# Kernel tuning notes

Hardware: AMD Instinct MI355X
Metric: run time of the kernel (lower is better)

Reference implementation:

```python
import jax, jax.numpy as jnp
import numpy as np

B, S, H = 2, 2048, 2048
NH, NKV, HD = 32, 8, 64
ROPE_THETA = 10000.0


def _rope_cos_sin(seq_len, head_dim, dtype):
    inv_freq = 1.0 / (ROPE_THETA ** (jnp.arange(0, head_dim, 2, dtype=jnp.float32) / head_dim))
    pos = jnp.arange(seq_len, dtype=jnp.float32)
    freqs = jnp.outer(pos, inv_freq)                 # [S, HD/2]
    emb = jnp.concatenate([freqs, freqs], axis=-1)   # [S, HD]
    return jnp.cos(emb).astype(dtype), jnp.sin(emb).astype(dtype)


def _rotate_half(x):
    x1, x2 = jnp.split(x, 2, axis=-1)
    return jnp.concatenate([-x2, x1], axis=-1)


def setup_inputs() -> dict:
    key = jax.random.key(0)
    ks = jax.random.split(key, 5)
    sc = 0.02
    return {
        'hidden_states': jax.random.normal(ks[0], (B, S, H), dtype=jnp.float32),
        'attention_mask': jnp.ones((B, S), dtype=jnp.int32),
        'Wq': jax.random.normal(ks[1], (H, NH * HD), dtype=jnp.float32) * sc,
        'Wk': jax.random.normal(ks[2], (H, NKV * HD), dtype=jnp.float32) * sc,
        'Wv': jax.random.normal(ks[3], (H, NKV * HD), dtype=jnp.float32) * sc,
        'Wo': jax.random.normal(ks[4], (NH * HD, H), dtype=jnp.float32) * sc,
    }


def reference(hidden_states, attention_mask, Wq, Wk, Wv, Wo):
    b, s, _ = hidden_states.shape
    n_rep = NH // NKV
    q = (hidden_states @ Wq).reshape(b, s, NH, HD).transpose(0, 2, 1, 3)    # [b,NH,s,d]
    k = (hidden_states @ Wk).reshape(b, s, NKV, HD).transpose(0, 2, 1, 3)   # [b,NKV,s,d]
    v = (hidden_states @ Wv).reshape(b, s, NKV, HD).transpose(0, 2, 1, 3)

    cos, sin = _rope_cos_sin(s, HD, q.dtype)          # [s, d]
    cos, sin = cos[None, None], sin[None, None]
    q = q * cos + _rotate_half(q) * sin
    k = k * cos + _rotate_half(k) * sin

    # repeat_kv
    k = jnp.repeat(k, n_rep, axis=1)                  # [b,NH,s,d]
    v = jnp.repeat(v, n_rep, axis=1)

    min_val = jnp.finfo(q.dtype).min
    causal = jnp.where(jnp.triu(jnp.ones((s, s), dtype=bool), k=1), min_val, 0.0).astype(q.dtype)
    mask = causal[None, None]                         # [1,1,s,s]
    pad = (attention_mask == 0)[:, None, None, :]     # [b,1,1,s]
    mask = jnp.where(pad, min_val, mask)              # [b,1,s,s]

    scale = 1.0 / jnp.sqrt(jnp.asarray(HD, dtype=q.dtype))
    scores = jnp.einsum('bhqd,bhkd->bhqk', q, k) * scale + mask
    attn = jax.nn.softmax(scores, axis=-1)
    out = jnp.einsum('bhqk,bhkd->bhqd', attn, v)      # [b,NH,s,d]
    out = out.transpose(0, 2, 1, 3).reshape(b, s, NH * HD)
    return out @ Wo
```

## Files before the change

kernel.cpp:

```cpp
#include <hip/hip_runtime.h>
#include <hip/hip_bf16.h>
#include <math.h>

#define B_   2
#define S_   2048
#define H_   2048
#define NH_  32
#define NKV_ 8
#define HD_  64
#define M_   (B_*S_)
#define QCOLS (NH_*HD_)
#define KVCOLS (NKV_*HD_)

typedef __bf16 bf16x8 __attribute__((ext_vector_type(8)));
typedef short  short8_t __attribute__((ext_vector_type(8)));
typedef float  f32x4 __attribute__((ext_vector_type(4)));
typedef float  f32x16 __attribute__((ext_vector_type(16)));

__device__ __forceinline__ short f2bf(float f) {
  __hip_bfloat16 h = __float2bfloat16(f);
  union { __hip_bfloat16 h; short s; } u; u.h = h; return u.s;
}
__device__ __forceinline__ float bf2f(short s) {
  union { short s; __hip_bfloat16 h; } u; u.s = s;
  return __bfloat162float(u.h);
}

__device__ __forceinline__ unsigned cvt_pk_bf16(float a, float b) {
  unsigned r;
  asm("v_cvt_pk_bf16_f32 %0, %1, %2" : "=v"(r) : "v"(a), "v"(b));
  return r;
}

__device__ __forceinline__ void gload_lds16(const void* g, void* l) {
  __builtin_amdgcn_global_load_lds(
      (const __attribute__((address_space(1))) unsigned int*)g,
      (__attribute__((address_space(3))) unsigned int*)l, 16, 0, 0);
}


__global__ void convert_x_kernel(const float4* __restrict__ in, short* __restrict__ out, int n4) {
  int i = blockIdx.x * blockDim.x + threadIdx.x;
  if (i >= n4) return;
  float4 v = in[i];
  short4 o;
  o.x = f2bf(v.x); o.y = f2bf(v.y); o.z = f2bf(v.z); o.w = f2bf(v.w);
  *reinterpret_cast<short4*>(out + (size_t)i * 4) = o;
}

__global__ __launch_bounds__(256) void wtrans_kernel(const float* __restrict__ W,
                                                     short* __restrict__ Wt,
                                                     int K, int N) {
  __shared__ float tile[32][33];
  int n0 = blockIdx.x * 32, k0 = blockIdx.y * 32;
  int tx = threadIdx.x & 31, ty = threadIdx.x >> 5;
  #pragma unroll
  for (int j = 0; j < 32; j += 8)
    tile[ty + j][tx] = W[(size_t)(k0 + ty + j) * N + n0 + tx];
  __syncthreads();
  #pragma unroll
  for (int j = 0; j < 32; j += 8)
    Wt[(size_t)(n0 + ty + j) * K + k0 + tx] = f2bf(tile[tx][ty + j]);
}

__global__ void sincos_kernel(float2* __restrict__ tab) {
  int i = blockIdx.x * blockDim.x + threadIdx.x;
  int pos = i >> 5, f = i & 31;
  float inv = powf(10000.0f, -(float)f * (1.0f / 32.0f));
  float ang = (float)pos * inv;
  float s, c;
  sincosf(ang, &s, &c);
  tab[i] = make_float2(c, s);
}

template <int OUT_MODE>
__global__ __launch_bounds__(256, 2)
void gemm_db_kernel(const short* __restrict__ A, const short* __restrict__ Bt,
                    void* __restrict__ Cout, short* __restrict__ Vout,
                    const float2* __restrict__ tab, int M, int N, int K) {
  __shared__ short As[2][128 * 64];
  __shared__ short Bs[2][128 * 64];
  const int tid = threadIdx.x;
  const int lane = tid & 63, wave = tid >> 6;
  const int m0 = blockIdx.x * 128, n0 = blockIdx.y * 128;
  const int wm = (wave >> 1) * 64, wn = (wave & 1) * 64;
  const int lr = lane & 15, lk = (lane >> 4) * 8;
  const int srow = lane >> 3;
  const int scol = 8 * ((lane & 7) ^ srow);

  f32x4 acc[4][4];
  const f32x4 z = {0.f, 0.f, 0.f, 0.f};
  #pragma unroll
  for (int i = 0; i < 4; ++i)
    #pragma unroll
    for (int j = 0; j < 4; ++j) acc[i][j] = z;

  const int nt = K >> 6;

  auto stage = [&](int t, int buf) {
    const int kt = t << 6;
    #pragma unroll
    for (int i = 0; i < 4; ++i) {
      int chunk = wave * 4 + i;
      int row = chunk * 8 + srow;
      gload_lds16(&A[(size_t)(m0 + row) * K + kt + scol], &As[buf][chunk * 512]);
      gload_lds16(&Bt[(size_t)(n0 + row) * K + kt + scol], &Bs[buf][chunk * 512]);
    }
  };

  stage(0, 0);
  stage(1, 1);
  asm volatile("s_waitcnt vmcnt(8)" ::: "memory");
  __builtin_amdgcn_s_barrier();

  int aoff[4], boff[4];
  #pragma unroll
  for (int i = 0; i < 4; ++i) {
    int ra = wm + i * 16 + lr;
    int rb = wn + i * 16 + lr;
    aoff[i] = ra * 64 + (lk ^ ((ra & 7) << 3));
    boff[i] = rb * 64 + (lk ^ ((rb & 7) << 3));
  }

  for (int t = 0; t < nt; ++t) {
    const short* as = As[t & 1];
    const short* bs = Bs[t & 1];
    bf16x8 af[2][4], bfr[2][4];
    #pragma unroll
    for (int kh = 0; kh < 2; ++kh) {
      #pragma unroll
      for (int mi = 0; mi < 4; ++mi)
        af[kh][mi] = *reinterpret_cast<const bf16x8*>(&as[aoff[mi] ^ (kh * 32)]);
      #pragma unroll
      for (int ni = 0; ni < 4; ++ni)
        bfr[kh][ni] = *reinterpret_cast<const bf16x8*>(&bs[boff[ni] ^ (kh * 32)]);
    }
    #pragma unroll
    for (int kh = 0; kh < 2; ++kh)
      #pragma unroll
      for (int mi = 0; mi < 4; ++mi)
        #pragma unroll
        for (int ni = 0; ni < 4; ++ni)
          acc[mi][ni] = __builtin_amdgcn_mfma_f32_16x16x32_bf16(
              af[kh][mi], bfr[kh][ni], acc[mi][ni], 0, 0, 0);

    asm volatile("s_waitcnt lgkmcnt(0)" ::: "memory");
    __builtin_amdgcn_s_barrier();
    if (t + 2 < nt) {
      stage(t + 2, t & 1);
      asm volatile("s_waitcnt vmcnt(8)" ::: "memory");
    } else {
      asm volatile("s_waitcnt vmcnt(0)" ::: "memory");
    }
    __builtin_amdgcn_s_barrier();
  }

  const int r0 = (lane >> 4) * 4, cc = lane & 15;

  if (OUT_MODE == 1) {
    #pragma unroll
    for (int mi = 0; mi < 4; ++mi)
      #pragma unroll
      for (int ni = 0; ni < 4; ++ni)
        #pragma unroll
        for (int r = 0; r < 4; ++r) {
          int row = m0 + wm + mi * 16 + r0 + r;
          int col = n0 + wn + ni * 16 + cc;
          ((float*)Cout)[(size_t)row * N + col] = acc[mi][ni][r];
        }
  }

  if (OUT_MODE == 3) {
    #pragma unroll
    for (int mi = 0; mi < 4; ++mi)
      #pragma unroll
      for (int ni = 0; ni < 2; ++ni)
        #pragma unroll
        for (int r = 0; r < 4; ++r) {
          int row = m0 + wm + mi * 16 + r0 + r;
          int pos = row & (S_ - 1);
          int i = ni * 16 + cc;
          float2 cs = tab[pos * 32 + i];
          float a = acc[mi][ni][r], b = acc[mi][ni + 2][r];
          int col = n0 + wn + i;
          ((short*)Cout)[(size_t)row * QCOLS + col]      = f2bf((a * cs.x - b * cs.y) * 0.125f);
          ((short*)Cout)[(size_t)row * QCOLS + col + 32] = f2bf((b * cs.x + a * cs.y) * 0.125f);
        }
  }

  if (OUT_MODE == 5) {
    if (n0 + wn < 512) {
      #pragma unroll
      for (int mi = 0; mi < 4; ++mi)
        #pragma unroll
        for (int ni = 0; ni < 2; ++ni)
          #pragma unroll
          for (int r = 0; r < 4; ++r) {
            int row = m0 + wm + mi * 16 + r0 + r;
            int pos = row & (S_ - 1);
            int i = ni * 16 + cc;
            float2 cs = tab[pos * 32 + i];
            float a = acc[mi][ni][r], b = acc[mi][ni + 2][r];
            int col = n0 + wn + i;
            ((short*)Cout)[(size_t)row * KVCOLS + col]      = f2bf(a * cs.x - b * cs.y);
            ((short*)Cout)[(size_t)row * KVCOLS + col + 32] = f2bf(b * cs.x + a * cs.y);
          }
    } else {
      #pragma unroll
      for (int mi = 0; mi < 4; ++mi)
        #pragma unroll
        for (int ni = 0; ni < 4; ++ni) {
          int colv = n0 + wn + ni * 16 + cc - 512;
          int kvh = colv >> 6, d = colv & 63;
          int rowb = m0 + wm + mi * 16 + r0;
          int bb = rowb >> 11, s0 = rowb & (S_ - 1);
          short4 pk;
          pk.x = f2bf(acc[mi][ni][0]); pk.y = f2bf(acc[mi][ni][1]);
          pk.z = f2bf(acc[mi][ni][2]); pk.w = f2bf(acc[mi][ni][3]);
          *reinterpret_cast<short4*>(
              &Vout[(((size_t)(bb * NKV_ + kvh)) * 64 + d) * S_ + s0]) = pk;
        }
    }
  }
}

__global__ __launch_bounds__(512, 2)
void attn4_kernel(const short* __restrict__ Q, const short* __restrict__ Kc,
                  const short* __restrict__ Vtg, short* __restrict__ AO) {
  __shared__ short Ks[2][64 * 64];
  __shared__ short Vs[2][64 * 64];
  const int qt = (int)(gridDim.x - 1) - (int)blockIdx.x;
  const int h = blockIdx.y, b = blockIdx.z;
  const int hk = h >> 2;
  const int tid = threadIdx.x, lane = tid & 63, wave = tid >> 6;
  const int q0 = qt * 256;
  const int qw0 = q0 + wave * 32;
  const int l31 = lane & 31, l5 = lane >> 5;

  const short* Kbase = Kc + ((size_t)b * S_) * KVCOLS + hk * HD_;
  const short* Vbase = Vtg + ((size_t)(b * NKV_ + hk) * HD_) * S_;

  bf16x8 qf[4];
  {
    const short* qrow = Q + ((size_t)(b * S_ + qw0 + l31)) * QCOLS + h * HD_;
    #pragma unroll
    for (int kk = 0; kk < 4; ++kk)
      qf[kk] = *reinterpret_cast<const bf16x8*>(qrow + kk * 16 + l5 * 8);
  }

  const int r8 = lane >> 3;
  const int c8s = ((lane & 7) ^ r8) * 8;
  auto stageKV = [&](int t, int buf) {
    int row = wave * 8 + r8;
    gload_lds16(Kbase + (size_t)(t * 64 + row) * KVCOLS + c8s, &Ks[buf][wave * 512]);
    gload_lds16(Vbase + (size_t)row * S_ + t * 64 + c8s, &Vs[buf][wave * 512]);
  };

  f32x16 o0, o1;
  #pragma unroll
  for (int e = 0; e < 16; ++e) { o0[e] = 0.f; o1[e] = 0.f; }
  float lsum = 0.f;

  const int nt = qt * 4 + 4;
  const int rowx = (l31 & 7);

  stageKV(0, 0);
  stageKV(1, 1);
  asm volatile("s_waitcnt vmcnt(2)" ::: "memory");
  __builtin_amdgcn_s_barrier();

  for (int t = 0; t < nt; ++t) {
    const short* ks = Ks[t & 1];
    const short* vs = Vs[t & 1];
    const bool active = (t * 64 <= qw0 + 31);

    if (active) {
      f32x16 sa[2];
      #pragma unroll
      for (int e = 0; e < 16; ++e) { sa[0][e] = 0.f; sa[1][e] = 0.f; }
      #pragma unroll
      for (int kk = 0; kk < 4; ++kk) {
        int c8 = ((2 * kk + l5) ^ rowx) * 8;
        bf16x8 k0 = *reinterpret_cast<const bf16x8*>(&ks[l31 * 64 + c8]);
        bf16x8 k1 = *reinterpret_cast<const bf16x8*>(&ks[(32 + l31) * 64 + c8]);
        sa[0] = __builtin_amdgcn_mfma_f32_32x32x16_bf16(k0, qf[kk], sa[0], 0, 0, 0);
        sa[1] = __builtin_amdgcn_mfma_f32_32x32x16_bf16(k1, qf[kk], sa[1], 0, 0, 0);
      }

      const int qglob = qw0 + l31;
      const bool maskT = (t * 64 + 63 > qw0);
      #pragma unroll
      for (int kvt = 0; kvt < 2; ++kvt)
        #pragma unroll
        for (int e = 0; e < 16; ++e) {
          float p = __expf(sa[kvt][e]);
          if (maskT) {
            int gkv = t * 64 + kvt * 32 + (e & 3) + 8 * (e >> 2) + 4 * l5;
            p = (gkv <= qglob) ? p : 0.f;
          }
          sa[kvt][e] = p;
          lsum += p;
        }

      int4 pfrag[4];
      #pragma unroll
      for (int kvt = 0; kvt < 2; ++kvt)
        #pragma unroll
        for (int hh = 0; hh < 2; ++hh) {
          unsigned A0 = cvt_pk_bf16(sa[kvt][8 * hh + 0], sa[kvt][8 * hh + 1]);
          unsigned A1 = cvt_pk_bf16(sa[kvt][8 * hh + 2], sa[kvt][8 * hh + 3]);
          unsigned B0 = cvt_pk_bf16(sa[kvt][8 * hh + 4], sa[kvt][8 * hh + 5]);
          unsigned B1 = cvt_pk_bf16(sa[kvt][8 * hh + 6], sa[kvt][8 * hh + 7]);
          auto ra = __builtin_amdgcn_permlane32_swap(A0, B0, false, false);
          auto rb = __builtin_amdgcn_permlane32_swap(A1, B1, false, false);
          pfrag[kvt * 2 + hh] = make_int4((int)ra[0], (int)rb[0], (int)ra[1], (int)rb[1]);
        }

      #pragma unroll
      for (int kk = 0; kk < 4; ++kk) {
        bf16x8 pf = *reinterpret_cast<const bf16x8*>(&pfrag[kk]);
        int c8 = ((2 * kk + l5) ^ rowx) * 8;
        bf16x8 v0 = *reinterpret_cast<const bf16x8*>(&vs[l31 * 64 + c8]);
        bf16x8 v1 = *reinterpret_cast<const bf16x8*>(&vs[(32 + l31) * 64 + c8]);
        o0 = __builtin_amdgcn_mfma_f32_32x32x16_bf16(pf, v0, o0, 0, 0, 0);
        o1 = __builtin_amdgcn_mfma_f32_32x32x16_bf16(pf, v1, o1, 0, 0, 0);
      }
    }

    asm volatile("s_waitcnt lgkmcnt(0)" ::: "memory");
    __builtin_amdgcn_s_barrier();
    if (t + 2 < nt) {
      stageKV(t + 2, t & 1);
      asm volatile("s_waitcnt vmcnt(2)" ::: "memory");
    } else {
      asm volatile("s_waitcnt vmcnt(0)" ::: "memory");
    }
    __builtin_amdgcn_s_barrier();
  }

  float lt = lsum + __shfl_xor(lsum, 32, 64);
  float inv = 1.f / lt;
  #pragma unroll
  for (int e = 0; e < 16; ++e) {
    int qrow = (e & 3) + 8 * (e >> 2) + 4 * l5;
    float ir = __shfl(inv, qrow, 64);
    int qg = q0 + wave * 32 + qrow;
    size_t rbase = ((size_t)(b * S_ + qg)) * QCOLS + h * HD_;
    AO[rbase + l31]      = f2bf(o0[e] * ir);
    AO[rbase + 32 + l31] = f2bf(o1[e] * ir);
  }
}


extern "C" void kernel_launch(void* const* d_in, const int* in_sizes, int n_in,
                              void* d_out, int out_size, void* d_ws, size_t ws_size,
                              hipStream_t stream) {
  (void)in_sizes; (void)n_in; (void)out_size; (void)ws_size;
  const float* X  = (const float*)d_in[0];
  const float* Wq = (const float*)d_in[2];
  const float* Wk = (const float*)d_in[3];
  const float* Wv = (const float*)d_in[4];
  const float* Wo = (const float*)d_in[5];

  char* ws = (char*)d_ws;
  short* Xb   = (short*)ws;                ws += (size_t)M_ * H_ * 2;
  short* Wqt  = (short*)ws;                ws += (size_t)QCOLS * H_ * 2;
  short* Wkvt = (short*)ws;                ws += (size_t)2 * KVCOLS * H_ * 2;
  short* Wot  = (short*)ws;                ws += (size_t)H_ * QCOLS * 2;
  short* Qb   = (short*)ws;                ws += (size_t)M_ * QCOLS * 2;
  short* Kb   = (short*)ws;                ws += (size_t)M_ * KVCOLS * 2;
  short* Vtg  = (short*)ws;                ws += (size_t)M_ * KVCOLS * 2;
  short* AOb  = (short*)ws;                ws += (size_t)M_ * QCOLS * 2;
  float2* tab = (float2*)ws;               ws += (size_t)S_ * 32 * sizeof(float2);

  {
    int n4 = (M_ * H_) / 4;
    convert_x_kernel<<<n4 / 256, 256, 0, stream>>>((const float4*)X, Xb, n4);
  }
  wtrans_kernel<<<dim3(QCOLS / 32, H_ / 32), 256, 0, stream>>>(Wq, Wqt, H_, QCOLS);
  wtrans_kernel<<<dim3(KVCOLS / 32, H_ / 32), 256, 0, stream>>>(Wk, Wkvt, H_, KVCOLS);
  wtrans_kernel<<<dim3(KVCOLS / 32, H_ / 32), 256, 0, stream>>>(Wv, Wkvt + (size_t)KVCOLS * H_, H_, KVCOLS);
  wtrans_kernel<<<dim3(QCOLS / 32, H_ / 32), 256, 0, stream>>>(Wo, Wot, H_, QCOLS);
  sincos_kernel<<<(S_ * 32) / 256, 256, 0, stream>>>(tab);
  gemm_db_kernel<3><<<dim3(M_ / 128, QCOLS / 128), 256, 0, stream>>>(
      Xb, Wqt, Qb, nullptr, tab, M_, QCOLS, H_);
  gemm_db_kernel<5><<<dim3(M_ / 128, (2 * KVCOLS) / 128), 256, 0, stream>>>(
      Xb, Wkvt, Kb, Vtg, tab, M_, 2 * KVCOLS, H_);
  attn4_kernel<<<dim3(S_ / 256, NH_, B_), 512, 0, stream>>>(Qb, Kb, Vtg, AOb);
  gemm_db_kernel<1><<<dim3(M_ / 128, H_ / 128), 256, 0, stream>>>(
      AOb, Wot, (float*)d_out, nullptr, nullptr, M_, H_, QCOLS);
}
```

Before: 327.2 us.

## Fuse QKV projections into one GEMM and pair causal query tiles per attention block

The Q, K and V projections now run as one GEMM over a concatenated transposed weight matrix. The epilogue routes each column range to the scaled-RoPE Q, RoPE K or transposed V output, which removes a launch and the wave-quantization tail of the small KV GEMM. The attention kernel processes two query tiles per block (tile i and tile 7-i), so every block does the same causal work and each K/V tile staged in shared memory serves both. In exchange the attention kernel holds twice the accumulators and query fragments in registers, which may cut occupancy, and it launches half as many blocks.

After: 302.9 us. 1.08x faster.

```diff
diff --git a/kernel.cpp b/kernel.cpp
--- a/kernel.cpp
+++ b/kernel.cpp
@@ -21,10 +21,6 @@
   __hip_bfloat16 h = __float2bfloat16(f);
   union { __hip_bfloat16 h; short s; } u; u.h = h; return u.s;
 }
-__device__ __forceinline__ float bf2f(short s) {
-  union { short s; __hip_bfloat16 h; } u; u.s = s;
-  return __bfloat162float(u.h);
-}
 
 __device__ __forceinline__ unsigned cvt_pk_bf16(float a, float b) {
   unsigned r;
@@ -76,7 +72,8 @@
 template <int OUT_MODE>
 __global__ __launch_bounds__(256, 2)
 void gemm_db_kernel(const short* __restrict__ A, const short* __restrict__ Bt,
-                    void* __restrict__ Cout, short* __restrict__ Vout,
+                    void* __restrict__ Cout, short* __restrict__ Kout,
+                    short* __restrict__ Vout,
                     const float2* __restrict__ tab, int M, int N, int K) {
   __shared__ short As[2][128 * 64];
   __shared__ short Bs[2][128 * 64];
@@ -170,26 +167,9 @@
         }
   }
 
-  if (OUT_MODE == 3) {
-    #pragma unroll
-    for (int mi = 0; mi < 4; ++mi)
-      #pragma unroll
-      for (int ni = 0; ni < 2; ++ni)
-        #pragma unroll
-        for (int r = 0; r < 4; ++r) {
-          int row = m0 + wm + mi * 16 + r0 + r;
-          int pos = row & (S_ - 1);
-          int i = ni * 16 + cc;
-          float2 cs = tab[pos * 32 + i];
-          float a = acc[mi][ni][r], b = acc[mi][ni + 2][r];
-          int col = n0 + wn + i;
-          ((short*)Cout)[(size_t)row * QCOLS + col]      = f2bf((a * cs.x - b * cs.y) * 0.125f);
-          ((short*)Cout)[(size_t)row * QCOLS + col + 32] = f2bf((b * cs.x + a * cs.y) * 0.125f);
-        }
-  }
-
-  if (OUT_MODE == 5) {
-    if (n0 + wn < 512) {
+  if (OUT_MODE == 7) {
+    const int chunk = n0 + wn;
+    if (chunk < 2048) {
       #pragma unroll
       for (int mi = 0; mi < 4; ++mi)
         #pragma unroll
@@ -201,16 +181,32 @@
             int i = ni * 16 + cc;
             float2 cs = tab[pos * 32 + i];
             float a = acc[mi][ni][r], b = acc[mi][ni + 2][r];
-            int col = n0 + wn + i;
-            ((short*)Cout)[(size_t)row * KVCOLS + col]      = f2bf(a * cs.x - b * cs.y);
-            ((short*)Cout)[(size_t)row * KVCOLS + col + 32] = f2bf(b * cs.x + a * cs.y);
+            int col = chunk + i;
+            ((short*)Cout)[(size_t)row * QCOLS + col]      = f2bf((a * cs.x - b * cs.y) * 0.125f);
+            ((short*)Cout)[(size_t)row * QCOLS + col + 32] = f2bf((b * cs.x + a * cs.y) * 0.125f);
+          }
+    } else if (chunk < 2560) {
+      #pragma unroll
+      for (int mi = 0; mi < 4; ++mi)
+        #pragma unroll
+        for (int ni = 0; ni < 2; ++ni)
+          #pragma unroll
+          for (int r = 0; r < 4; ++r) {
+            int row = m0 + wm + mi * 16 + r0 + r;
+            int pos = row & (S_ - 1);
+            int i = ni * 16 + cc;
+            float2 cs = tab[pos * 32 + i];
+            float a = acc[mi][ni][r], b = acc[mi][ni + 2][r];
+            int col = chunk - 2048 + i;
+            Kout[(size_t)row * KVCOLS + col]      = f2bf(a * cs.x - b * cs.y);
+            Kout[(size_t)row * KVCOLS + col + 32] = f2bf(b * cs.x + a * cs.y);
           }
     } else {
       #pragma unroll
       for (int mi = 0; mi < 4; ++mi)
         #pragma unroll
         for (int ni = 0; ni < 4; ++ni) {
-          int colv = n0 + wn + ni * 16 + cc - 512;
+          int colv = chunk + ni * 16 + cc - 2560;
           int kvh = colv >> 6, d = colv & 63;
           int rowb = m0 + wm + mi * 16 + r0;
           int bb = rowb >> 11, s0 = rowb & (S_ - 1);
@@ -224,28 +220,78 @@
   }
 }
 
+__device__ __forceinline__ void softmax_pack(f32x16* sa, int qw0, int t, int l31, int l5,
+                                             float& lsum, int4* pfrag) {
+  const int qglob = qw0 + l31;
+  const bool maskT = (t * 64 + 63 > qw0);
+  #pragma unroll
+  for (int kvt = 0; kvt < 2; ++kvt)
+    #pragma unroll
+    for (int e = 0; e < 16; ++e) {
+      float p = __expf(sa[kvt][e]);
+      if (maskT) {
+        int gkv = t * 64 + kvt * 32 + (e & 3) + 8 * (e >> 2) + 4 * l5;
+        p = (gkv <= qglob) ? p : 0.f;
+      }
+      sa[kvt][e] = p;
+      lsum += p;
+    }
+  #pragma unroll
+  for (int kvt = 0; kvt < 2; ++kvt)
+    #pragma unroll
+    for (int hh = 0; hh < 2; ++hh) {
+      unsigned A0 = cvt_pk_bf16(sa[kvt][8 * hh + 0], sa[kvt][8 * hh + 1]);
+      unsigned A1 = cvt_pk_bf16(sa[kvt][8 * hh + 2], sa[kvt][8 * hh + 3]);
+      unsigned B0 = cvt_pk_bf16(sa[kvt][8 * hh + 4], sa[kvt][8 * hh + 5]);
+      unsigned B1 = cvt_pk_bf16(sa[kvt][8 * hh + 6], sa[kvt][8 * hh + 7]);
+      auto ra = __builtin_amdgcn_permlane32_swap(A0, B0, false, false);
+      auto rb = __builtin_amdgcn_permlane32_swap(A1, B1, false, false);
+      pfrag[kvt * 2 + hh] = make_int4((int)ra[0], (int)rb[0], (int)ra[1], (int)rb[1]);
+    }
+}
+
+__device__ __forceinline__ void store_O(short* __restrict__ AO, const f32x16& o0,
+                                        const f32x16& o1, float lsum, int qw0,
+                                        int b, int h, int l31, int l5) {
+  float lt = lsum + __shfl_xor(lsum, 32, 64);
+  float inv = 1.f / lt;
+  #pragma unroll
+  for (int e = 0; e < 16; ++e) {
+    int qrow = (e & 3) + 8 * (e >> 2) + 4 * l5;
+    float ir = __shfl(inv, qrow, 64);
+    int qg = qw0 + qrow;
+    size_t rbase = ((size_t)(b * S_ + qg)) * QCOLS + h * HD_;
+    AO[rbase + l31]      = f2bf(o0[e] * ir);
+    AO[rbase + 32 + l31] = f2bf(o1[e] * ir);
+  }
+}
+
 __global__ __launch_bounds__(512, 2)
-void attn4_kernel(const short* __restrict__ Q, const short* __restrict__ Kc,
+void attn5_kernel(const short* __restrict__ Q, const short* __restrict__ Kc,
                   const short* __restrict__ Vtg, short* __restrict__ AO) {
   __shared__ short Ks[2][64 * 64];
   __shared__ short Vs[2][64 * 64];
-  const int qt = (int)(gridDim.x - 1) - (int)blockIdx.x;
+  const int qtA = blockIdx.x;
+  const int qtB = 7 - qtA;
   const int h = blockIdx.y, b = blockIdx.z;
   const int hk = h >> 2;
   const int tid = threadIdx.x, lane = tid & 63, wave = tid >> 6;
-  const int q0 = qt * 256;
-  const int qw0 = q0 + wave * 32;
   const int l31 = lane & 31, l5 = lane >> 5;
+  const int qwA0 = qtA * 256 + wave * 32;
+  const int qwB0 = qtB * 256 + wave * 32;
 
   const short* Kbase = Kc + ((size_t)b * S_) * KVCOLS + hk * HD_;
   const short* Vbase = Vtg + ((size_t)(b * NKV_ + hk) * HD_) * S_;
 
-  bf16x8 qf[4];
+  bf16x8 qfA[4], qfB[4];
   {
-    const short* qrow = Q + ((size_t)(b * S_ + qw0 + l31)) * QCOLS + h * HD_;
-    #pragma unroll
-    for (int kk = 0; kk < 4; ++kk)
-      qf[kk] = *reinterpret_cast<const bf16x8*>(qrow + kk * 16 + l5 * 8);
+    const short* qa = Q + ((size_t)(b * S_ + qwA0 + l31)) * QCOLS + h * HD_;
+    const short* qb = Q + ((size_t)(b * S_ + qwB0 + l31)) * QCOLS + h * HD_;
+    #pragma unroll
+    for (int kk = 0; kk < 4; ++kk) {
+      qfA[kk] = *reinterpret_cast<const bf16x8*>(qa + kk * 16 + l5 * 8);
+      qfB[kk] = *reinterpret_cast<const bf16x8*>(qb + kk * 16 + l5 * 8);
+    }
   }
 
   const int r8 = lane >> 3;
@@ -256,80 +302,73 @@
     gload_lds16(Vbase + (size_t)row * S_ + t * 64 + c8s, &Vs[buf][wave * 512]);
   };
 
-  f32x16 o0, o1;
-  #pragma unroll
-  for (int e = 0; e < 16; ++e) { o0[e] = 0.f; o1[e] = 0.f; }
-  float lsum = 0.f;
-
-  const int nt = qt * 4 + 4;
-  const int rowx = (l31 & 7);
+  f32x16 oA0, oA1, oB0, oB1;
+  #pragma unroll
+  for (int e = 0; e < 16; ++e) { oA0[e] = 0.f; oA1[e] = 0.f; oB0[e] = 0.f; oB1[e] = 0.f; }
+  float lsA = 0.f, lsB = 0.f;
+
+  const int ntB = 4 * qtB + 4;
+  const int rowx = l31 & 7;
 
   stageKV(0, 0);
   stageKV(1, 1);
   asm volatile("s_waitcnt vmcnt(2)" ::: "memory");
   __builtin_amdgcn_s_barrier();
 
-  for (int t = 0; t < nt; ++t) {
+  for (int t = 0; t < ntB; ++t) {
     const short* ks = Ks[t & 1];
     const short* vs = Vs[t & 1];
-    const bool active = (t * 64 <= qw0 + 31);
-
-    if (active) {
-      f32x16 sa[2];
-      #pragma unroll
-      for (int e = 0; e < 16; ++e) { sa[0][e] = 0.f; sa[1][e] = 0.f; }
-      #pragma unroll
-      for (int kk = 0; kk < 4; ++kk) {
-        int c8 = ((2 * kk + l5) ^ rowx) * 8;
-        bf16x8 k0 = *reinterpret_cast<const bf16x8*>(&ks[l31 * 64 + c8]);
-        bf16x8 k1 = *reinterpret_cast<const bf16x8*>(&ks[(32 + l31) * 64 + c8]);
-        sa[0] = __builtin_amdgcn_mfma_f32_32x32x16_bf16(k0, qf[kk], sa[0], 0, 0, 0);
-        sa[1] = __builtin_amdgcn_mfma_f32_32x32x16_bf16(k1, qf[kk], sa[1], 0, 0, 0);
+    const bool actA = (t * 64 <= qwA0 + 31);
+    const bool actB = (t * 64 <= qwB0 + 31);
+
+    f32x16 saA[2], saB[2];
+    if (actA) {
+      #pragma unroll
+      for (int e = 0; e < 16; ++e) { saA[0][e] = 0.f; saA[1][e] = 0.f; }
+    }
+    if (actB) {
+      #pragma unroll
+      for (int e = 0; e < 16; ++e) { saB[0][e] = 0.f; saB[1][e] = 0.f; }
+    }
+    #pragma unroll
+    for (int kk = 0; kk < 4; ++kk) {
+      int c8 = ((2 * kk + l5) ^ rowx) * 8;
+      bf16x8 k0 = *reinterpret_cast<const bf16x8*>(&ks[l31 * 64 + c8]);
+      bf16x8 k1 = *reinterpret_cast<const bf16x8*>(&ks[(32 + l31) * 64 + c8]);
+      if (actA) {
+        saA[0] = __builtin_amdgcn_mfma_f32_32x32x16_bf16(k0, qfA[kk], saA[0], 0, 0, 0);
+        saA[1] = __builtin_amdgcn_mfma_f32_32x32x16_bf16(k1, qfA[kk], saA[1], 0, 0, 0);
       }
-
-      const int qglob = qw0 + l31;
-      const bool maskT = (t * 64 + 63 > qw0);
-      #pragma unroll
-      for (int kvt = 0; kvt < 2; ++kvt)
-        #pragma unroll
-        for (int e = 0; e < 16; ++e) {
-          float p = __expf(sa[kvt][e]);
-          if (maskT) {
-            int gkv = t * 64 + kvt * 32 + (e & 3) + 8 * (e >> 2) + 4 * l5;
-            p = (gkv <= qglob) ? p : 0.f;
-          }
-          sa[kvt][e] = p;
-          lsum += p;
-        }
-
-      int4 pfrag[4];
-      #pragma unroll
-      for (int kvt = 0; kvt < 2; ++kvt)
-        #pragma unroll
-        for (int hh = 0; hh < 2; ++hh) {
-          unsigned A0 = cvt_pk_bf16(sa[kvt][8 * hh + 0], sa[kvt][8 * hh + 1]);
-          unsigned A1 = cvt_pk_bf16(sa[kvt][8 * hh + 2], sa[kvt][8 * hh + 3]);
-          unsigned B0 = cvt_pk_bf16(sa[kvt][8 * hh + 4], sa[kvt][8 * hh + 5]);
-          unsigned B1 = cvt_pk_bf16(sa[kvt][8 * hh + 6], sa[kvt][8 * hh + 7]);
-          auto ra = __builtin_amdgcn_permlane32_swap(A0, B0, false, false);
-          auto rb = __builtin_amdgcn_permlane32_swap(A1, B1, false, false);
-          pfrag[kvt * 2 + hh] = make_int4((int)ra[0], (int)rb[0], (int)ra[1], (int)rb[1]);
-        }
-
-      #pragma unroll
-      for (int kk = 0; kk < 4; ++kk) {
-        bf16x8 pf = *reinterpret_cast<const bf16x8*>(&pfrag[kk]);
-        int c8 = ((2 * kk + l5) ^ rowx) * 8;
-        bf16x8 v0 = *reinterpret_cast<const bf16x8*>(&vs[l31 * 64 + c8]);
-        bf16x8 v1 = *reinterpret_cast<const bf16x8*>(&vs[(32 + l31) * 64 + c8]);
-        o0 = __builtin_amdgcn_mfma_f32_32x32x16_bf16(pf, v0, o0, 0, 0, 0);
-        o1 = __builtin_amdgcn_mfma_f32_32x32x16_bf16(pf, v1, o1, 0, 0, 0);
+      if (actB) {
+        saB[0] = __builtin_amdgcn_mfma_f32_32x32x16_bf16(k0, qfB[kk], saB[0], 0, 0, 0);
+        saB[1] = __builtin_amdgcn_mfma_f32_32x32x16_bf16(k1, qfB[kk], saB[1], 0, 0, 0);
+      }
+    }
+
+    int4 pfA[4], pfB[4];
+    if (actA) softmax_pack(saA, qwA0, t, l31, l5, lsA, pfA);
+    if (actB) softmax_pack(saB, qwB0, t, l31, l5, lsB, pfB);
+
+    #pragma unroll
+    for (int kk = 0; kk < 4; ++kk) {
+      int c8 = ((2 * kk + l5) ^ rowx) * 8;
+      bf16x8 v0 = *reinterpret_cast<const bf16x8*>(&vs[l31 * 64 + c8]);
+      bf16x8 v1 = *reinterpret_cast<const bf16x8*>(&vs[(32 + l31) * 64 + c8]);
+      if (actA) {
+        bf16x8 pf = *reinterpret_cast<const bf16x8*>(&pfA[kk]);
+        oA0 = __builtin_amdgcn_mfma_f32_32x32x16_bf16(pf, v0, oA0, 0, 0, 0);
+        oA1 = __builtin_amdgcn_mfma_f32_32x32x16_bf16(pf, v1, oA1, 0, 0, 0);
+      }
+      if (actB) {
+        bf16x8 pf = *reinterpret_cast<const bf16x8*>(&pfB[kk]);
+        oB0 = __builtin_amdgcn_mfma_f32_32x32x16_bf16(pf, v0, oB0, 0, 0, 0);
+        oB1 = __builtin_amdgcn_mfma_f32_32x32x16_bf16(pf, v1, oB1, 0, 0, 0);
       }
     }
 
     asm volatile("s_waitcnt lgkmcnt(0)" ::: "memory");
     __builtin_amdgcn_s_barrier();
-    if (t + 2 < nt) {
+    if (t + 2 < ntB) {
       stageKV(t + 2, t & 1);
       asm volatile("s_waitcnt vmcnt(2)" ::: "memory");
     } else {
@@ -338,17 +377,8 @@
     __builtin_amdgcn_s_barrier();
   }
 
-  float lt = lsum + __shfl_xor(lsum, 32, 64);
-  float inv = 1.f / lt;
-  #pragma unroll
-  for (int e = 0; e < 16; ++e) {
-    int qrow = (e & 3) + 8 * (e >> 2) + 4 * l5;
-    float ir = __shfl(inv, qrow, 64);
-    int qg = q0 + wave * 32 + qrow;
-    size_t rbase = ((size_t)(b * S_ + qg)) * QCOLS + h * HD_;
-    AO[rbase + l31]      = f2bf(o0[e] * ir);
-    AO[rbase + 32 + l31] = f2bf(o1[e] * ir);
-  }
+  store_O(AO, oA0, oA1, lsA, qtA * 256 + wave * 32, b, h, l31, l5);
+  store_O(AO, oB0, oB1, lsB, qtB * 256 + wave * 32, b, h, l31, l5);
 }
 
 
@@ -363,30 +393,29 @@
   const float* Wo = (const float*)d_in[5];
 
   char* ws = (char*)d_ws;
-  short* Xb   = (short*)ws;                ws += (size_t)M_ * H_ * 2;
-  short* Wqt  = (short*)ws;                ws += (size_t)QCOLS * H_ * 2;
-  short* Wkvt = (short*)ws;                ws += (size_t)2 * KVCOLS * H_ * 2;
-  short* Wot  = (short*)ws;                ws += (size_t)H_ * QCOLS * 2;
-  short* Qb   = (short*)ws;                ws += (size_t)M_ * QCOLS * 2;
-  short* Kb   = (short*)ws;                ws += (size_t)M_ * KVCOLS * 2;
-  short* Vtg  = (short*)ws;                ws += (size_t)M_ * KVCOLS * 2;
-  short* AOb  = (short*)ws;                ws += (size_t)M_ * QCOLS * 2;
-  float2* tab = (float2*)ws;               ws += (size_t)S_ * 32 * sizeof(float2);
+  short* Xb    = (short*)ws;               ws += (size_t)M_ * H_ * 2;
+  short* Wqkvt = (short*)ws;               ws += (size_t)3072 * H_ * 2;
+  short* Wot   = (short*)ws;               ws += (size_t)H_ * QCOLS * 2;
+  short* Qb    = (short*)ws;               ws += (size_t)M_ * QCOLS * 2;
+  short* Kb    = (short*)ws;               ws += (size_t)M_ * KVCOLS * 2;
+  short* Vtg   = (short*)ws;               ws += (size_t)M_ * KVCOLS * 2;
+  short* AOb   = (short*)ws;               ws += (size_t)M_ * QCOLS * 2;
+  float2* tab  = (float2*)ws;              ws += (size_t)S_ * 32 * sizeof(float2);
 
   {
     int n4 = (M_ * H_) / 4;
     convert_x_kernel<<<n4 / 256, 256, 0, stream>>>((const float4*)X, Xb, n4);
   }
-  wtrans_kernel<<<dim3(QCOLS / 32, H_ / 32), 256, 0, stream>>>(Wq, Wqt, H_, QCOLS);
-  wtrans_kernel<<<dim3(KVCOLS / 32, H_ / 32), 256, 0, stream>>>(Wk, Wkvt, H_, KVCOLS);
-  wtrans_kernel<<<dim3(KVCOLS / 32, H_ / 32), 256, 0, stream>>>(Wv, Wkvt + (size_t)KVCOLS * H_, H_, KVCOLS);
+  wtrans_kernel<<<dim3(QCOLS / 32, H_ / 32), 256, 0, stream>>>(Wq, Wqkvt, H_, QCOLS);
+  wtrans_kernel<<<dim3(KVCOLS / 32, H_ / 32), 256, 0, stream>>>(
+      Wk, Wqkvt + (size_t)2048 * H_, H_, KVCOLS);
+  wtrans_kernel<<<dim3(KVCOLS / 32, H_ / 32), 256, 0, stream>>>(
+      Wv, Wqkvt + (size_t)2560 * H_, H_, KVCOLS);
   wtrans_kernel<<<dim3(QCOLS / 32, H_ / 32), 256, 0, stream>>>(Wo, Wot, H_, QCOLS);
   sincos_kernel<<<(S_ * 32) / 256, 256, 0, stream>>>(tab);
-  gemm_db_kernel<3><<<dim3(M_ / 128, QCOLS / 128), 256, 0, stream>>>(
-      Xb, Wqt, Qb, nullptr, tab, M_, QCOLS, H_);
-  gemm_db_kernel<5><<<dim3(M_ / 128, (2 * KVCOLS) / 128), 256, 0, stream>>>(
-      Xb, Wkvt, Kb, Vtg, tab, M_, 2 * KVCOLS, H_);
-  attn4_kernel<<<dim3(S_ / 256, NH_, B_), 512, 0, stream>>>(Qb, Kb, Vtg, AOb);
+  gemm_db_kernel<7><<<dim3(M_ / 128, 3072 / 128), 256, 0, stream>>>(
+      Xb, Wqkvt, Qb, Kb, Vtg, tab, M_, 3072, H_);
+  attn5_kernel<<<dim3(4, NH_, B_), 512, 0, stream>>>(Qb, Kb, Vtg, AOb);
   gemm_db_kernel<1><<<dim3(M_ / 128, H_ / 128), 256, 0, stream>>>(
-      AOb, Wot, (float*)d_out, nullptr, nullptr, M_, H_, QCOLS);
-}
+      AOb, Wot, (float*)d_out, nullptr, nullptr, nullptr, M_, H_, QCOLS);
+}
```
